# Kernel tuning notes

Hardware: AMD Instinct MI355X
Metric: run time of the kernel (lower is better)

Reference implementation:

```python
import jax, jax.numpy as jnp
import numpy as np

B, T, D, H = 4, 2048, 1024, 16
HD = D // H  # head dim = 64


def setup_inputs() -> dict:
    key = jax.random.key(0)
    ks = jax.random.split(key, 6)
    s = 0.02
    return {
        "x": jax.random.normal(ks[0], (B, T, D), dtype=jnp.float32),
        "Wk": jax.random.normal(ks[1], (D, D), dtype=jnp.float32) * s,
        "Wq": jax.random.normal(ks[2], (D, D), dtype=jnp.float32) * s,
        "Wv": jax.random.normal(ks[3], (D, D), dtype=jnp.float32) * s,
        "Wp": jax.random.normal(ks[4], (D, D), dtype=jnp.float32) * s,
        "bp": jnp.zeros((D,), dtype=jnp.float32),
    }


def reference(x, Wk, Wq, Wv, Wp, bp):
    # nn.Linear applies x @ W.T; weights here are stored torch-style [out, in]
    Bq, Tq, _ = x.shape
    k = (x @ Wk.T).reshape(Bq, Tq, H, HD).transpose(0, 2, 1, 3)  # [B,H,T,hd]
    q = (x @ Wq.T).reshape(Bq, Tq, H, HD).transpose(0, 2, 1, 3)
    v = (x @ Wv.T).reshape(Bq, Tq, H, HD).transpose(0, 2, 1, 3)
    scale = HD ** -0.5
    attn = jnp.einsum('bhqd,bhkd->bhqk', q, k) * scale  # [B,H,T,T]
    causal = jnp.tril(jnp.ones((Tq, Tq), dtype=bool))
    attn = jnp.where(causal, attn, -jnp.inf)
    attn = jax.nn.softmax(attn, axis=-1)
    # dropout p=0.0 -> identity (eval semantics)
    out = jnp.einsum('bhqk,bhkd->bhqd', attn, v)  # [B,H,T,hd]
    out = out.transpose(0, 2, 1, 3).reshape(Bq, Tq, D)
    return out @ Wp.T + bp
```

## Files before the change

### kernel.cpp

```cpp
#include <hip/hip_runtime.h>
#include <hip/hip_bf16.h>
#include <stdint.h>


typedef __bf16 bf16x8 __attribute__((ext_vector_type(8)));
typedef float floatx4 __attribute__((ext_vector_type(4)));
typedef unsigned short ushort_t;
typedef unsigned short ushortx8 __attribute__((ext_vector_type(8)));
typedef unsigned short ushortx4 __attribute__((ext_vector_type(4)));
typedef short shortx4 __attribute__((ext_vector_type(4)));

#define MFMA16(a, b, c) __builtin_amdgcn_mfma_f32_16x16x32_bf16((a), (b), (c), 0, 0, 0)
#define MFMA16K16(a, b, c) __builtin_amdgcn_mfma_f32_16x16x16bf16_1k((a), (b), (c), 0, 0, 0)
#define EXP2F(x) __builtin_amdgcn_exp2f(x)

static __device__ __forceinline__ ushort_t f2bfu(float f) {
  union { float f; unsigned u; } v; v.f = f;
  unsigned r = v.u + 0x7FFFu + ((v.u >> 16) & 1u);
  return (ushort_t)(r >> 16);
}

static __device__ __forceinline__ unsigned pack_bf2(float lo, float hi) {
  return __builtin_amdgcn_perm(__float_as_uint(hi), __float_as_uint(lo), 0x07060302);
}

static __device__ __forceinline__ void gl_lds16(const void* g, void* l) {
  __builtin_amdgcn_global_load_lds(
      (const __attribute__((address_space(1))) void*)g,
      (__attribute__((address_space(3))) void*)l, 16, 0, 0);
}

__global__ void cvt_all(const float* __restrict__ x,  const float* __restrict__ wk,
                        const float* __restrict__ wq, const float* __restrict__ wv,
                        const float* __restrict__ wp, ushortx4* __restrict__ dst) {
  const int i = blockIdx.x * blockDim.x + threadIdx.x;
  const float4* src; int off;
  if (i < 2097152) { src = (const float4*)x; off = i; }
  else {
    const int r = i - 2097152;
    const int sel = r >> 18;
    off = r & 262143;
    src = (const float4*)(sel == 0 ? wk : sel == 1 ? wq : sel == 2 ? wv : wp);
  }
  const float4 f = src[off];
  ushortx4 o;
  o[0] = f2bfu(f.x); o[1] = f2bfu(f.y); o[2] = f2bfu(f.z); o[3] = f2bfu(f.w);
  dst[i] = o;
}

__global__ __launch_bounds__(256) void gemm_qkv(
    const ushort_t* __restrict__ X,
    const ushort_t* __restrict__ Wq, const ushort_t* __restrict__ Wk,
    const ushort_t* __restrict__ Wv,
    ushort_t* __restrict__ qb, ushort_t* __restrict__ kb, ushort_t* __restrict__ vtb)
{
  const int L = (int)(blockIdx.x + 64 * (blockIdx.y + 8 * blockIdx.z));
  const int rr = L & 7, mm = L >> 3;
  const int m0 = (rr + 8 * (mm & 7)) * 128;
  const int rest = mm >> 3;
  const int n0 = (rest & 7) * 128;
  const int z = rest >> 3;

  const ushort_t* Bm = (z == 0) ? Wq : (z == 1) ? Wk : Wv;
  __shared__ ushort_t Al[128 * 64];
  __shared__ ushort_t Bl[128 * 64];
  const int tid = threadIdx.x;
  const int w = tid >> 6, lane = tid & 63, g = lane >> 4, c = lane & 15;
  const int wm = w >> 1, wn = w & 1;
  const int cswz = c & 7;

  floatx4 acc[4][4];
  const floatx4 zero4 = {0.f, 0.f, 0.f, 0.f};
#pragma unroll
  for (int i = 0; i < 4; ++i)
#pragma unroll
    for (int j = 0; j < 4; ++j) acc[i][j] = zero4;

  const int srow = tid >> 3;
  const int gsw  = ((tid & 7) ^ (srow & 7)) * 8;

  for (int k0 = 0; k0 < 1024; k0 += 64) {
#pragma unroll
    for (int p = 0; p < 4; ++p) {
      const int row = p * 32 + srow;
      gl_lds16(&X [(size_t)(m0 + row) * 1024 + k0 + gsw], &Al[p * 2048 + tid * 8]);
      gl_lds16(&Bm[(size_t)(n0 + row) * 1024 + k0 + gsw], &Bl[p * 2048 + tid * 8]);
    }
    __syncthreads();
#pragma unroll
    for (int kk = 0; kk < 2; ++kk) {
      bf16x8 af[4], bfr[4];
#pragma unroll
      for (int i = 0; i < 4; ++i) {
        const int sw = ((kk * 4 + g) ^ cswz) * 8;
        af[i]  = *reinterpret_cast<const bf16x8*>(&Al[(wm * 64 + i * 16 + c) * 64 + sw]);
        bfr[i] = *reinterpret_cast<const bf16x8*>(&Bl[(wn * 64 + i * 16 + c) * 64 + sw]);
      }
#pragma unroll
      for (int i = 0; i < 4; ++i)
#pragma unroll
        for (int j = 0; j < 4; ++j)
          acc[i][j] = MFMA16(af[i], bfr[j], acc[i][j]);
    }
    __syncthreads();
  }

#pragma unroll
  for (int i = 0; i < 4; ++i) {
#pragma unroll
    for (int j = 0; j < 4; ++j) {
      const int mbase = m0 + wm * 64 + i * 16 + g * 4;
      const int n = n0 + wn * 64 + j * 16 + c;
      const int h = n >> 6, d = n & 63;
      if (z == 2) {
        const int bb = mbase >> 11, t = mbase & 2047;
        ushortx4 pk;
#pragma unroll
        for (int r = 0; r < 4; ++r) pk[r] = f2bfu(acc[i][j][r]);
        *reinterpret_cast<ushortx4*>(&vtb[(size_t)((bb * 16 + h) * 64 + d) * 2048 + t]) = pk;
      } else {
        ushort_t* ob = (z == 0) ? qb : kb;
#pragma unroll
        for (int r = 0; r < 4; ++r) {
          const int m = mbase + r;
          const int bb = m >> 11, t = m & 2047;
          ob[(size_t)((bb * 16 + h) * 2048 + t) * 64 + d] = f2bfu(acc[i][j][r]);
        }
      }
    }
  }
}

__global__ __launch_bounds__(256, 4) void attn_kernel(
    const ushort_t* __restrict__ qbuf, const ushort_t* __restrict__ kbuf,
    const ushort_t* __restrict__ vtbuf, ushort_t* __restrict__ obuf)
{
  const int L = (int)(blockIdx.x + 16 * (blockIdx.y + 16 * blockIdx.z));
  const int rr = L & 7, mm = L >> 3;
  const int j = mm >> 3;
  const int bhl = rr * 8 + (mm & 7);
  const int h = bhl & 15, b = bhl >> 4;

  const int tid = threadIdx.x, w = tid >> 6, lane = tid & 63, g = lane >> 4, c = lane & 15;

  __shared__ ushort_t Kl[128 * 64];
  __shared__ ushort_t Vl[64 * 128];

  const size_t bh = (size_t)(b * 16 + h);
  const ushort_t* kb_bh = kbuf + bh * 2048 * 64;
  const ushort_t* vt_bh = vtbuf + bh * 64 * 2048;
  const ushort_t* qb_bh = qbuf + bh * 2048 * 64;

  const int rb0 = j * 64 + w * 16;
  const int rb1 = (31 - j) * 64 + w * 16;

  bf16x8 aq0[2], aq1[2];
  {
    const ushort_t* qp0 = qb_bh + (size_t)(rb0 + c) * 64;
    aq0[0] = *reinterpret_cast<const bf16x8*>(qp0 + g * 8);
    aq0[1] = *reinterpret_cast<const bf16x8*>(qp0 + 32 + g * 8);
    const ushort_t* qp1 = qb_bh + (size_t)(rb1 + c) * 64;
    aq1[0] = *reinterpret_cast<const bf16x8*>(qp1 + g * 8);
    aq1[1] = *reinterpret_cast<const bf16x8*>(qp1 + 32 + g * 8);
  }

  floatx4 oacc0[4], oacc1[4];
  float l0 = 0.f, l1 = 0.f;
  const floatx4 zero4 = {0.f, 0.f, 0.f, 0.f};
#pragma unroll
  for (int td = 0; td < 4; ++td) { oacc0[td] = zero4; oacc1[td] = zero4; }

  const int krow_s = tid >> 3;
  const int kgsw   = ((tid & 7) ^ (krow_s & 7)) * 8;
  const int vrow_s = tid >> 4;
  const int vgsw   = ((tid & 15) ^ (vrow_s & 15)) * 8;

  const float SCALE = 0.18033688011112042f;

  const int n128 = (33 - j) >> 1;
  for (int kt = 0; kt < n128; ++kt) {
    const int key0 = kt * 128;
#pragma unroll
    for (int p = 0; p < 4; ++p) {
      const int kr = p * 32 + krow_s;
      gl_lds16(&kb_bh[(size_t)(key0 + kr) * 64 + kgsw], &Kl[p * 2048 + tid * 8]);
      const int vr = p * 16 + vrow_s;
      gl_lds16(&vt_bh[(size_t)vr * 2048 + key0 + vgsw], &Vl[p * 2048 + tid * 8]);
    }
    __syncthreads();

#pragma unroll
    for (int s = 0; s < 2; ++s) {
      const int ti = 2 * kt + s;
      const int key0s = ti * 64;
#pragma unroll
      for (int grp = 0; grp < 2; ++grp) {
        const int lim = (grp == 0) ? j : 31 - j;
        if (ti > lim) continue;
        const int rb = (grp == 0) ? rb0 : rb1;
        const bf16x8 b0 = (grp == 0) ? aq0[0] : aq1[0];
        const bf16x8 b1 = (grp == 0) ? aq0[1] : aq1[1];

        float pv[4][4];
#pragma unroll
        for (int t4 = 0; t4 < 4; ++t4) {
          const int krow = s * 64 + t4 * 16 + c;
          const bf16x8 k0f = *reinterpret_cast<const bf16x8*>(&Kl[krow * 64 + ((g) ^ (c & 7)) * 8]);
          const bf16x8 k1f = *reinterpret_cast<const bf16x8*>(&Kl[krow * 64 + ((4 + g) ^ (c & 7)) * 8]);
          floatx4 sa = zero4;
          sa = MFMA16(k0f, b0, sa);
          sa = MFMA16(k1f, b1, sa);
          if (ti == lim) {
            const int q = rb + c;
#pragma unroll
            for (int r = 0; r < 4; ++r) {
              const int key = key0s + t4 * 16 + g * 4 + r;
              const float e = EXP2F(sa[r] * SCALE);
              pv[t4][r] = (key <= q) ? e : 0.f;
            }
          } else {
#pragma unroll
            for (int r = 0; r < 4; ++r) pv[t4][r] = EXP2F(sa[r] * SCALE);
          }
        }
        float lsum = 0.f;
#pragma unroll
        for (int t4 = 0; t4 < 4; ++t4)
          lsum += (pv[t4][0] + pv[t4][1]) + (pv[t4][2] + pv[t4][3]);
        if (grp == 0) l0 += lsum; else l1 += lsum;

#pragma unroll
        for (int t4 = 0; t4 < 4; ++t4) {
          union { unsigned u[2]; shortx4 v; } pk;
          pk.u[0] = pack_bf2(pv[t4][0], pv[t4][1]);
          pk.u[1] = pack_bf2(pv[t4][2], pv[t4][3]);
          const int cc = s * 8 + t4 * 2 + (g >> 1);
          const int ko = (g & 1) * 4;
#pragma unroll
          for (int td = 0; td < 4; ++td) {
            const shortx4 va = *reinterpret_cast<const shortx4*>(
                &Vl[(td * 16 + c) * 128 + (cc ^ c) * 8 + ko]);
            if (grp == 0) oacc0[td] = MFMA16K16(va, pk.v, oacc0[td]);
            else          oacc1[td] = MFMA16K16(va, pk.v, oacc1[td]);
          }
        }
      }
    }
    __syncthreads();
  }

#pragma unroll
  for (int grp = 0; grp < 2; ++grp) {
    float ls = (grp == 0) ? l0 : l1;
    ls += __shfl_xor(ls, 16, 64);
    ls += __shfl_xor(ls, 32, 64);
    const float inv = 1.f / ls;
    const int q = ((grp == 0) ? rb0 : rb1) + c;
    ushort_t* ob = &obuf[((size_t)(b * 2048 + q) * 16 + h) * 64];
#pragma unroll
    for (int td = 0; td < 4; ++td) {
      const floatx4 oa = (grp == 0) ? oacc0[td] : oacc1[td];
      ushortx4 pk;
#pragma unroll
      for (int r = 0; r < 4; ++r) pk[r] = f2bfu(oa[r] * inv);
      *reinterpret_cast<ushortx4*>(&ob[td * 16 + g * 4]) = pk;
    }
  }
}

__global__ __launch_bounds__(256) void gemm_proj(
    const ushort_t* __restrict__ A, const ushort_t* __restrict__ Wp,
    const float* __restrict__ bias, float* __restrict__ out)
{
  const int L = (int)(blockIdx.x + 64 * blockIdx.y);
  const int rr = L & 7, mm = L >> 3;
  const int m0 = (rr + 8 * (mm & 7)) * 128;
  const int n0 = (mm >> 3) * 128;

  __shared__ ushort_t Al[128 * 64];
  __shared__ ushort_t Bl[128 * 64];
  const int tid = threadIdx.x;
  const int w = tid >> 6, lane = tid & 63, g = lane >> 4, c = lane & 15;
  const int wm = w >> 1, wn = w & 1;
  const int cswz = c & 7;

  floatx4 acc[4][4];
  const floatx4 zero4 = {0.f, 0.f, 0.f, 0.f};
#pragma unroll
  for (int i = 0; i < 4; ++i)
#pragma unroll
    for (int j = 0; j < 4; ++j) acc[i][j] = zero4;

  const int srow = tid >> 3;
  const int gsw  = ((tid & 7) ^ (srow & 7)) * 8;

  for (int k0 = 0; k0 < 1024; k0 += 64) {
#pragma unroll
    for (int p = 0; p < 4; ++p) {
      const int row = p * 32 + srow;
      gl_lds16(&A [(size_t)(m0 + row) * 1024 + k0 + gsw], &Al[p * 2048 + tid * 8]);
      gl_lds16(&Wp[(size_t)(n0 + row) * 1024 + k0 + gsw], &Bl[p * 2048 + tid * 8]);
    }
    __syncthreads();
#pragma unroll
    for (int kk = 0; kk < 2; ++kk) {
      bf16x8 af[4], bfr[4];
#pragma unroll
      for (int i = 0; i < 4; ++i) {
        const int sw = ((kk * 4 + g) ^ cswz) * 8;
        af[i]  = *reinterpret_cast<const bf16x8*>(&Al[(wm * 64 + i * 16 + c) * 64 + sw]);
        bfr[i] = *reinterpret_cast<const bf16x8*>(&Bl[(wn * 64 + i * 16 + c) * 64 + sw]);
      }
#pragma unroll
      for (int i = 0; i < 4; ++i)
#pragma unroll
        for (int j = 0; j < 4; ++j)
          acc[i][j] = MFMA16(af[i], bfr[j], acc[i][j]);
    }
    __syncthreads();
  }

#pragma unroll
  for (int i = 0; i < 4; ++i) {
#pragma unroll
    for (int j = 0; j < 4; ++j) {
      const int n = n0 + wn * 64 + j * 16 + c;
      const float bv = bias[n];
#pragma unroll
      for (int r = 0; r < 4; ++r) {
        const int m = m0 + wm * 64 + i * 16 + g * 4 + r;
        out[(size_t)m * 1024 + n] = acc[i][j][r] + bv;
      }
    }
  }
}

extern "C" void kernel_launch(void* const* d_in, const int* in_sizes, int n_in,
                              void* d_out, int out_size, void* d_ws, size_t ws_size,
                              hipStream_t stream) {
  const float* x  = (const float*)d_in[0];
  const float* Wk = (const float*)d_in[1];
  const float* Wq = (const float*)d_in[2];
  const float* Wv = (const float*)d_in[3];
  const float* Wp = (const float*)d_in[4];
  const float* bp = (const float*)d_in[5];
  float* out = (float*)d_out;

  char* ws = (char*)d_ws;
  const size_t SZ_X = (size_t)8192 * 1024 * 2;
  const size_t SZ_W = (size_t)1024 * 1024 * 2;
  ushort_t* xb    = (ushort_t*)ws;  ws += SZ_X;
  ushort_t* wkb   = (ushort_t*)ws;  ws += SZ_W;
  ushort_t* wqb   = (ushort_t*)ws;  ws += SZ_W;
  ushort_t* wvb   = (ushort_t*)ws;  ws += SZ_W;
  ushort_t* wpb   = (ushort_t*)ws;  ws += SZ_W;
  ushort_t* qbuf  = (ushort_t*)ws;  ws += SZ_X;
  ushort_t* kbuf  = (ushort_t*)ws;  ws += SZ_X;
  ushort_t* vtbuf = (ushort_t*)ws;  ws += SZ_X;
  ushort_t* obuf  = xb;

  cvt_all<<<12288, 256, 0, stream>>>(x, Wk, Wq, Wv, Wp, (ushortx4*)xb);

  gemm_qkv<<<dim3(64, 8, 3), 256, 0, stream>>>(xb, wqb, wkb, wvb, qbuf, kbuf, vtbuf);
  attn_kernel<<<dim3(16, 16, 4), 256, 0, stream>>>(qbuf, kbuf, vtbuf, obuf);
  gemm_proj<<<dim3(64, 8), 256, 0, stream>>>(obuf, wpb, bp, out);
}
```

Before: 240.3 us.

## Use 256x256 double-buffered tiles with interleaved prefetch in QKV GEMM

The QKV projection GEMM moves from 128x128 tiles with 256 threads and a single LDS buffer to 256x256 tiles with 512 threads and double-buffered LDS. Loads for the next k-tile are spread across the MFMA phases and guarded with manual vmcnt waits and raw barriers, and s_setprio raises priority around MFMA bursts. The aim is to hide global-load latency and raise operand reuse per LDS read. In exchange it uses 128KB of LDS and more accumulator registers per thread, and launches only 384 blocks, which may leave some CUs underused.

```diff
diff --git a/kernel.cpp b/kernel.cpp
--- a/kernel.cpp
+++ b/kernel.cpp
@@ -48,68 +48,103 @@
   dst[i] = o;
 }
 
-__global__ __launch_bounds__(256) void gemm_qkv(
+__global__ __launch_bounds__(512, 2) void gemm_qkv(
     const ushort_t* __restrict__ X,
     const ushort_t* __restrict__ Wq, const ushort_t* __restrict__ Wk,
     const ushort_t* __restrict__ Wv,
     ushort_t* __restrict__ qb, ushort_t* __restrict__ kb, ushort_t* __restrict__ vtb)
 {
-  const int L = (int)(blockIdx.x + 64 * (blockIdx.y + 8 * blockIdx.z));
+  const int L = (int)blockIdx.x;
   const int rr = L & 7, mm = L >> 3;
-  const int m0 = (rr + 8 * (mm & 7)) * 128;
-  const int rest = mm >> 3;
-  const int n0 = (rest & 7) * 128;
-  const int z = rest >> 3;
+  const int m0 = (rr + 8 * (mm & 3)) * 256;
+  const int rest = mm >> 2;
+  const int n0 = (rest & 3) * 256;
+  const int z = rest >> 2;
 
   const ushort_t* Bm = (z == 0) ? Wq : (z == 1) ? Wk : Wv;
-  __shared__ ushort_t Al[128 * 64];
-  __shared__ ushort_t Bl[128 * 64];
+
+  __shared__ ushort_t As0[256 * 64];
+  __shared__ ushort_t As1[256 * 64];
+  __shared__ ushort_t Bs0[256 * 64];
+  __shared__ ushort_t Bs1[256 * 64];
+
   const int tid = threadIdx.x;
   const int w = tid >> 6, lane = tid & 63, g = lane >> 4, c = lane & 15;
-  const int wm = w >> 1, wn = w & 1;
+  const int wm = w >> 2, wn = w & 3;
   const int cswz = c & 7;
 
-  floatx4 acc[4][4];
+  floatx4 acc[8][4];
   const floatx4 zero4 = {0.f, 0.f, 0.f, 0.f};
 #pragma unroll
-  for (int i = 0; i < 4; ++i)
+  for (int i = 0; i < 8; ++i)
 #pragma unroll
     for (int j = 0; j < 4; ++j) acc[i][j] = zero4;
 
   const int srow = tid >> 3;
   const int gsw  = ((tid & 7) ^ (srow & 7)) * 8;
 
-  for (int k0 = 0; k0 < 1024; k0 += 64) {
-#pragma unroll
-    for (int p = 0; p < 4; ++p) {
-      const int row = p * 32 + srow;
-      gl_lds16(&X [(size_t)(m0 + row) * 1024 + k0 + gsw], &Al[p * 2048 + tid * 8]);
-      gl_lds16(&Bm[(size_t)(n0 + row) * 1024 + k0 + gsw], &Bl[p * 2048 + tid * 8]);
-    }
-    __syncthreads();
-#pragma unroll
-    for (int kk = 0; kk < 2; ++kk) {
-      bf16x8 af[4], bfr[4];
-#pragma unroll
-      for (int i = 0; i < 4; ++i) {
-        const int sw = ((kk * 4 + g) ^ cswz) * 8;
-        af[i]  = *reinterpret_cast<const bf16x8*>(&Al[(wm * 64 + i * 16 + c) * 64 + sw]);
-        bfr[i] = *reinterpret_cast<const bf16x8*>(&Bl[(wn * 64 + i * 16 + c) * 64 + sw]);
+#pragma unroll
+  for (int p = 0; p < 4; ++p) {
+    gl_lds16(&X [(size_t)(m0 + p * 64 + srow) * 1024 + gsw], &As0[p * 4096 + tid * 8]);
+    gl_lds16(&Bm[(size_t)(n0 + p * 64 + srow) * 1024 + gsw], &Bs0[p * 4096 + tid * 8]);
+  }
+
+  auto ktile = [&](const ushort_t* __restrict__ Ac, const ushort_t* __restrict__ Bc,
+                   ushort_t* __restrict__ An, ushort_t* __restrict__ Bn,
+                   int kn, bool stagenext) {
+    if (stagenext) {
+      gl_lds16(&X [(size_t)(m0 + srow) * 1024 + kn + gsw], &An[tid * 8]);
+      gl_lds16(&Bm[(size_t)(n0 + srow) * 1024 + kn + gsw], &Bn[tid * 8]);
+      asm volatile("s_waitcnt vmcnt(2)" ::: "memory");
+    } else {
+      asm volatile("s_waitcnt vmcnt(0)" ::: "memory");
+    }
+    __builtin_amdgcn_s_barrier();
+
+    bf16x8 bfr[4][2];
+#pragma unroll
+    for (int j = 0; j < 4; ++j)
+#pragma unroll
+      for (int kk = 0; kk < 2; ++kk)
+        bfr[j][kk] = *reinterpret_cast<const bf16x8*>(
+            &Bc[(wn * 64 + j * 16 + c) * 64 + ((kk * 4 + g) ^ cswz) * 8]);
+
+#pragma unroll
+    for (int q = 0; q < 4; ++q) {
+      bf16x8 af[2][2];
+#pragma unroll
+      for (int ii = 0; ii < 2; ++ii)
+#pragma unroll
+        for (int kk = 0; kk < 2; ++kk)
+          af[ii][kk] = *reinterpret_cast<const bf16x8*>(
+              &Ac[(wm * 128 + (q * 2 + ii) * 16 + c) * 64 + ((kk * 4 + g) ^ cswz) * 8]);
+      if (q && stagenext) {
+        gl_lds16(&X [(size_t)(m0 + q * 64 + srow) * 1024 + kn + gsw], &An[q * 4096 + tid * 8]);
+        gl_lds16(&Bm[(size_t)(n0 + q * 64 + srow) * 1024 + kn + gsw], &Bn[q * 4096 + tid * 8]);
       }
-#pragma unroll
-      for (int i = 0; i < 4; ++i)
+      __builtin_amdgcn_s_setprio(1);
+#pragma unroll
+      for (int ii = 0; ii < 2; ++ii)
 #pragma unroll
         for (int j = 0; j < 4; ++j)
-          acc[i][j] = MFMA16(af[i], bfr[j], acc[i][j]);
-    }
-    __syncthreads();
-  }
-
-#pragma unroll
-  for (int i = 0; i < 4; ++i) {
+#pragma unroll
+          for (int kk = 0; kk < 2; ++kk)
+            acc[q * 2 + ii][j] = MFMA16(af[ii][kk], bfr[j][kk], acc[q * 2 + ii][j]);
+      __builtin_amdgcn_s_setprio(0);
+    }
+    __builtin_amdgcn_s_barrier();
+  };
+
+  for (int kt = 0; kt < 16; kt += 2) {
+    ktile(As0, Bs0, As1, Bs1, (kt + 1) * 64, true);
+    ktile(As1, Bs1, As0, Bs0, (kt + 2) * 64, kt < 14);
+  }
+
+#pragma unroll
+  for (int i = 0; i < 8; ++i) {
 #pragma unroll
     for (int j = 0; j < 4; ++j) {
-      const int mbase = m0 + wm * 64 + i * 16 + g * 4;
+      const int mbase = m0 + wm * 128 + i * 16 + g * 4;
       const int n = n0 + wn * 64 + j * 16 + c;
       const int h = n >> 6, d = n & 63;
       if (z == 2) {
@@ -361,7 +396,7 @@
 
   cvt_all<<<12288, 256, 0, stream>>>(x, Wk, Wq, Wv, Wp, (ushortx4*)xb);
 
-  gemm_qkv<<<dim3(64, 8, 3), 256, 0, stream>>>(xb, wqb, wkb, wvb, qbuf, kbuf, vtbuf);
+  gemm_qkv<<<dim3(384), 512, 0, stream>>>(xb, wqb, wkb, wvb, qbuf, kbuf, vtbuf);
   attn_kernel<<<dim3(16, 16, 4), 256, 0, stream>>>(qbuf, kbuf, vtbuf, obuf);
   gemm_proj<<<dim3(64, 8), 256, 0, stream>>>(obuf, wpb, bp, out);
 }
```

Measured after the change: 240.4 us. No clear change (+0.0%).

## Double-buffer K/V tiles in LDS to overlap loads with attention compute

Applied to the files above, without the earlier changes.

Replaces the single 128-key LDS tile with two 64-key buffers and prefetches the next tile asynchronously while computing the current one, using a partial vmcnt wait and raw barriers. The goal is to hide global-to-LDS load latency behind MFMA work instead of stalling at each synchronization point. It halves the work per barrier and adds more loop iterations. It also depends on the vmcnt count matching the number of outstanding loads.

```diff
diff --git a/kernel.cpp b/kernel.cpp
--- a/kernel.cpp
+++ b/kernel.cpp
@@ -143,8 +143,8 @@
 
   const int tid = threadIdx.x, w = tid >> 6, lane = tid & 63, g = lane >> 4, c = lane & 15;
 
-  __shared__ ushort_t Kl[128 * 64];
-  __shared__ ushort_t Vl[64 * 128];
+  __shared__ ushort_t Kl[2][64 * 64];
+  __shared__ ushort_t Vl[2][64 * 64];
 
   const size_t bh = (size_t)(b * 16 + h);
   const ushort_t* kb_bh = kbuf + bh * 2048 * 64;
@@ -170,83 +170,93 @@
 #pragma unroll
   for (int td = 0; td < 4; ++td) { oacc0[td] = zero4; oacc1[td] = zero4; }
 
-  const int krow_s = tid >> 3;
-  const int kgsw   = ((tid & 7) ^ (krow_s & 7)) * 8;
-  const int vrow_s = tid >> 4;
-  const int vgsw   = ((tid & 15) ^ (vrow_s & 15)) * 8;
+  const int srow8 = tid >> 3;
+  const int gswz  = ((tid & 7) ^ (srow8 & 7)) * 8;
 
   const float SCALE = 0.18033688011112042f;
 
-  const int n128 = (33 - j) >> 1;
-  for (int kt = 0; kt < n128; ++kt) {
-    const int key0 = kt * 128;
-#pragma unroll
-    for (int p = 0; p < 4; ++p) {
-      const int kr = p * 32 + krow_s;
-      gl_lds16(&kb_bh[(size_t)(key0 + kr) * 64 + kgsw], &Kl[p * 2048 + tid * 8]);
-      const int vr = p * 16 + vrow_s;
-      gl_lds16(&vt_bh[(size_t)vr * 2048 + key0 + vgsw], &Vl[p * 2048 + tid * 8]);
-    }
-    __syncthreads();
-
-#pragma unroll
-    for (int s = 0; s < 2; ++s) {
-      const int ti = 2 * kt + s;
-      const int key0s = ti * 64;
-#pragma unroll
-      for (int grp = 0; grp < 2; ++grp) {
-        const int lim = (grp == 0) ? j : 31 - j;
-        if (ti > lim) continue;
-        const int rb = (grp == 0) ? rb0 : rb1;
-        const bf16x8 b0 = (grp == 0) ? aq0[0] : aq1[0];
-        const bf16x8 b1 = (grp == 0) ? aq0[1] : aq1[1];
-
-        float pv[4][4];
-#pragma unroll
-        for (int t4 = 0; t4 < 4; ++t4) {
-          const int krow = s * 64 + t4 * 16 + c;
-          const bf16x8 k0f = *reinterpret_cast<const bf16x8*>(&Kl[krow * 64 + ((g) ^ (c & 7)) * 8]);
-          const bf16x8 k1f = *reinterpret_cast<const bf16x8*>(&Kl[krow * 64 + ((4 + g) ^ (c & 7)) * 8]);
-          floatx4 sa = zero4;
-          sa = MFMA16(k0f, b0, sa);
-          sa = MFMA16(k1f, b1, sa);
-          if (ti == lim) {
-            const int q = rb + c;
-#pragma unroll
-            for (int r = 0; r < 4; ++r) {
-              const int key = key0s + t4 * 16 + g * 4 + r;
-              const float e = EXP2F(sa[r] * SCALE);
-              pv[t4][r] = (key <= q) ? e : 0.f;
-            }
-          } else {
-#pragma unroll
-            for (int r = 0; r < 4; ++r) pv[t4][r] = EXP2F(sa[r] * SCALE);
+  const int NT = 32 - j;
+
+  auto stage = [&](int ti, int buf) {
+    const int key0 = ti * 64;
+#pragma unroll
+    for (int p = 0; p < 2; ++p) {
+      gl_lds16(&kb_bh[(size_t)(key0 + p * 32 + srow8) * 64 + gswz],
+               &Kl[buf][p * 2048 + tid * 8]);
+      gl_lds16(&vt_bh[(size_t)(p * 32 + srow8) * 2048 + key0 + gswz],
+               &Vl[buf][p * 2048 + tid * 8]);
+    }
+  };
+
+  stage(0, 0);
+
+  for (int ti = 0; ti < NT; ++ti) {
+    const int cur = ti & 1;
+    if (ti + 1 < NT) {
+      stage(ti + 1, cur ^ 1);
+      asm volatile("s_waitcnt vmcnt(4)" ::: "memory");
+    } else {
+      asm volatile("s_waitcnt vmcnt(0)" ::: "memory");
+    }
+    __builtin_amdgcn_s_barrier();
+
+    const ushort_t* Kc = Kl[cur];
+    const ushort_t* Vc = Vl[cur];
+    const int key0s = ti * 64;
+
+#pragma unroll
+    for (int grp = 0; grp < 2; ++grp) {
+      const int lim = (grp == 0) ? j : 31 - j;
+      if (ti > lim) continue;
+      const int rb = (grp == 0) ? rb0 : rb1;
+      const bf16x8 b0 = (grp == 0) ? aq0[0] : aq1[0];
+      const bf16x8 b1 = (grp == 0) ? aq0[1] : aq1[1];
+
+      float pv[4][4];
+#pragma unroll
+      for (int t4 = 0; t4 < 4; ++t4) {
+        const int krow = t4 * 16 + c;
+        const bf16x8 k0f = *reinterpret_cast<const bf16x8*>(&Kc[krow * 64 + ((g) ^ (c & 7)) * 8]);
+        const bf16x8 k1f = *reinterpret_cast<const bf16x8*>(&Kc[krow * 64 + ((4 + g) ^ (c & 7)) * 8]);
+        floatx4 sa = zero4;
+        sa = MFMA16(k0f, b0, sa);
+        sa = MFMA16(k1f, b1, sa);
+        if (ti == lim) {
+          const int q = rb + c;
+#pragma unroll
+          for (int r = 0; r < 4; ++r) {
+            const int key = key0s + t4 * 16 + g * 4 + r;
+            const float e = EXP2F(sa[r] * SCALE);
+            pv[t4][r] = (key <= q) ? e : 0.f;
           }
+        } else {
+#pragma unroll
+          for (int r = 0; r < 4; ++r) pv[t4][r] = EXP2F(sa[r] * SCALE);
         }
-        float lsum = 0.f;
-#pragma unroll
-        for (int t4 = 0; t4 < 4; ++t4)
-          lsum += (pv[t4][0] + pv[t4][1]) + (pv[t4][2] + pv[t4][3]);
-        if (grp == 0) l0 += lsum; else l1 += lsum;
-
-#pragma unroll
-        for (int t4 = 0; t4 < 4; ++t4) {
-          union { unsigned u[2]; shortx4 v; } pk;
-          pk.u[0] = pack_bf2(pv[t4][0], pv[t4][1]);
-          pk.u[1] = pack_bf2(pv[t4][2], pv[t4][3]);
-          const int cc = s * 8 + t4 * 2 + (g >> 1);
-          const int ko = (g & 1) * 4;
-#pragma unroll
-          for (int td = 0; td < 4; ++td) {
-            const shortx4 va = *reinterpret_cast<const shortx4*>(
-                &Vl[(td * 16 + c) * 128 + (cc ^ c) * 8 + ko]);
-            if (grp == 0) oacc0[td] = MFMA16K16(va, pk.v, oacc0[td]);
-            else          oacc1[td] = MFMA16K16(va, pk.v, oacc1[td]);
-          }
+      }
+      float lsum = 0.f;
+#pragma unroll
+      for (int t4 = 0; t4 < 4; ++t4)
+        lsum += (pv[t4][0] + pv[t4][1]) + (pv[t4][2] + pv[t4][3]);
+      if (grp == 0) l0 += lsum; else l1 += lsum;
+
+#pragma unroll
+      for (int t4 = 0; t4 < 4; ++t4) {
+        union { unsigned u[2]; shortx4 v; } pk;
+        pk.u[0] = pack_bf2(pv[t4][0], pv[t4][1]);
+        pk.u[1] = pack_bf2(pv[t4][2], pv[t4][3]);
+        const int cc = t4 * 2 + (g >> 1);
+        const int ko = (g & 1) * 4;
+#pragma unroll
+        for (int td = 0; td < 4; ++td) {
+          const shortx4 va = *reinterpret_cast<const shortx4*>(
+              &Vc[(td * 16 + c) * 64 + (cc ^ (c & 7)) * 8 + ko]);
+          if (grp == 0) oacc0[td] = MFMA16K16(va, pk.v, oacc0[td]);
+          else          oacc1[td] = MFMA16K16(va, pk.v, oacc1[td]);
         }
       }
     }
-    __syncthreads();
+    __builtin_amdgcn_s_barrier();
   }
 
 #pragma unroll
```

New measurement: 231.1 us (median of 2 runs). 1.04x faster.
